# Kernel optimization log

Measured on AMD Instinct MI355X. Metric: run time of the kernel, lower is better.

## Reference

```python
import jax, jax.numpy as jnp
import numpy as np
import math

B, S, D = 4, 2048, 1024


def setup_inputs() -> dict:
    key = jax.random.key(0)
    k1, k2, k3 = jax.random.split(key, 3)
    X = jax.random.normal(k1, (B, S, D), dtype=jnp.float32)
    # causal mask, broadcast over batch (True = keep)
    mask = jnp.broadcast_to(jnp.tril(jnp.ones((S, S), dtype=bool)), (B, S, S))
    # torch nn.Linear weights: y = x @ W.T; init scale ~ 1/sqrt(D)
    WQK = jax.random.normal(k2, (D, D), dtype=jnp.float32) / math.sqrt(D)
    WOV = jax.random.normal(k3, (D, D), dtype=jnp.float32) / math.sqrt(D)
    return {"X": X, "mask": mask, "WQK": WQK, "WOV": WOV}


def reference(X, mask, WQK, WOV):
    d = X.shape[-1]
    Q = jnp.einsum('bsd,ed->bse', X, WQK)          # WQK(X) = X @ WQK.T
    Sc = jnp.einsum('bse,bte->bst', Q, X)          # shared-QK scores: Q @ X^T
    # NOTE: original multiplies by sqrt(d_model) (not divide) - faithful
    Sc = Sc * jnp.asarray(math.sqrt(d), Sc.dtype)
    Sc = jnp.where(mask, Sc, -jnp.inf)
    A = jax.nn.softmax(Sc, axis=-1)                # dropout p=0.0 -> identity
    V = jnp.einsum('bsd,ed->bse', X, WOV)          # WOV(X)
    Y = jnp.einsum('bst,bte->bse', A, V)
    return (X + Y, A)
```

## Files before the change

### kernel.cpp

```cpp
#include <hip/hip_runtime.h>
#include <hip/hip_fp16.h>
#include <math.h>

typedef _Float16 half_t;
typedef _Float16 h8_t __attribute__((ext_vector_type(8)));
typedef _Float16 h4_t __attribute__((ext_vector_type(4)));
typedef float f4_t __attribute__((ext_vector_type(4)));

#define MFMA16(a, b, c) __builtin_amdgcn_mfma_f32_16x16x32_f16(a, b, c, 0, 0, 0)

static constexpr int kB = 4;
static constexpr int kS = 2048;
static constexpr int kD = 1024;
static constexpr int BM = 128;
static constexpr int BN = 128;
static constexpr int BK = 32;
static constexpr int NT = 512;

__device__ __forceinline__ void gload16(const half_t* g, half_t* l) {
  __builtin_amdgcn_global_load_lds(
      (const __attribute__((address_space(1))) void*)g,
      (__attribute__((address_space(3))) void*)l, 16, 0, 0);
}

__device__ __forceinline__ void stage_tile(half_t* __restrict__ sm,
                                           const half_t* __restrict__ g, int ld) {
  const int t = threadIdx.x;
  const int r = t >> 2;
  const int c = ((t & 3) * 8) ^ ((((r >> 1) & 3)) << 3);
  gload16(&g[(size_t)r * ld + c], &sm[r * BK + (t & 3) * 8]);
}

template <bool SPLIT>
__device__ __forceinline__ void stage_all(half_t* buf, const half_t* Ahi,
                                          const half_t* Alo, int lda,
                                          const half_t* Bhi, const half_t* Blo,
                                          int ldb, size_t ko) {
  stage_tile(buf, Ahi + ko, lda);
  stage_tile(buf + BM * BK, Bhi + ko, ldb);
  if (SPLIT) {
    stage_tile(buf + 2 * BM * BK, Alo + ko, lda);
    stage_tile(buf + 3 * BM * BK, Blo + ko, ldb);
  }
}

template <bool SPLIT>
__device__ __forceinline__ void gemm_core(const half_t* __restrict__ Ahi,
                                          const half_t* __restrict__ Alo, int lda,
                                          const half_t* __restrict__ Bhi,
                                          const half_t* __restrict__ Blo, int ldb,
                                          int k_iters, half_t* sm, f4_t acc[4][2]) {
  constexpr int BUFSZ = (SPLIT ? 4 : 2) * BM * BK;
  const int lane = threadIdx.x & 63;
  const int wid = threadIdx.x >> 6;
  const int wm = (wid >> 2) * 64;
  const int wn = (wid & 3) * 32;
  const int fr = lane & 15;
  const int fk = (((lane >> 4) * 8) ^ (((lane >> 1) & 3) << 3));

  half_t* cur = sm;
  half_t* nxt = sm + BUFSZ;

  stage_all<SPLIT>(cur, Ahi, Alo, lda, Bhi, Blo, ldb, 0);
  asm volatile("s_waitcnt vmcnt(0)" ::: "memory");
  __builtin_amdgcn_s_barrier();

  for (int kk = 0; kk < k_iters; ++kk) {
    if (kk + 1 < k_iters)
      stage_all<SPLIT>(nxt, Ahi, Alo, lda, Bhi, Blo, ldb, (size_t)(kk + 1) * BK);
    const half_t* sAh = cur;
    const half_t* sBh = cur + BM * BK;
    const half_t* sAl = cur + 2 * BM * BK;
    const half_t* sBl = cur + 3 * BM * BK;
    h8_t a[4], b[2], al[4], bl[2];
#pragma unroll
    for (int i = 0; i < 4; ++i) {
      a[i] = *(const h8_t*)&sAh[(wm + i * 16 + fr) * BK + fk];
      if (SPLIT) al[i] = *(const h8_t*)&sAl[(wm + i * 16 + fr) * BK + fk];
    }
#pragma unroll
    for (int j = 0; j < 2; ++j) {
      b[j] = *(const h8_t*)&sBh[(wn + j * 16 + fr) * BK + fk];
      if (SPLIT) bl[j] = *(const h8_t*)&sBl[(wn + j * 16 + fr) * BK + fk];
    }
#pragma unroll
    for (int i = 0; i < 4; ++i)
#pragma unroll
      for (int j = 0; j < 2; ++j) {
        acc[i][j] = MFMA16(a[i], b[j], acc[i][j]);
        if (SPLIT) {
          acc[i][j] = MFMA16(a[i], bl[j], acc[i][j]);
          acc[i][j] = MFMA16(al[i], b[j], acc[i][j]);
        }
      }
    asm volatile("s_waitcnt vmcnt(0)" ::: "memory");
    __builtin_amdgcn_s_barrier();
    half_t* t = cur; cur = nxt; nxt = t;
  }
}

__global__ __launch_bounds__(NT) void gemm_q_kernel(
    const half_t* __restrict__ Xhi, const half_t* __restrict__ Xlo,
    const half_t* __restrict__ Whi, const half_t* __restrict__ Wlo,
    half_t* __restrict__ Qhi, half_t* __restrict__ Qlo) {
  __shared__ half_t sm[2 * 4 * BM * BK];
  const size_t arow = (size_t)blockIdx.y * BM;
  const size_t brow = (size_t)blockIdx.x * BN;
  f4_t acc[4][2] = {};
  gemm_core<true>(Xhi + arow * kD, Xlo + arow * kD, kD,
                  Whi + brow * kD, Wlo + brow * kD, kD, kD / BK, sm, acc);
  const int lane = threadIdx.x & 63;
  const int wid = threadIdx.x >> 6;
  const int wm = (wid >> 2) * 64, wn = (wid & 3) * 32;
  const int c16 = lane & 15, r4 = (lane >> 4) * 4;
#pragma unroll
  for (int i = 0; i < 4; ++i)
#pragma unroll
    for (int j = 0; j < 2; ++j)
#pragma unroll
      for (int r = 0; r < 4; ++r) {
        const size_t row = arow + wm + i * 16 + r4 + r;
        const size_t col = brow + wn + j * 16 + c16;
        const float q = acc[i][j][r];
        const half_t qh = (half_t)q;
        const half_t ql = (half_t)(q - (float)qh);
        const size_t idx = row * kD + col;
        Qhi[idx] = qh;
        Qlo[idx] = ql;
      }
}

__global__ __launch_bounds__(NT) void gemm_v_kernel(
    const half_t* __restrict__ Xhi, const half_t* __restrict__ Whi,
    half_t* __restrict__ Vt) {
  __shared__ half_t sm[2 * 2 * BM * BK];
  const size_t arow = (size_t)blockIdx.y * BM;
  const size_t brow = (size_t)blockIdx.x * BN;
  f4_t acc[4][2] = {};
  gemm_core<false>(Xhi + arow * kD, nullptr, kD, Whi + brow * kD, nullptr, kD,
                   kD / BK, sm, acc);
  const int lane = threadIdx.x & 63;
  const int wid = threadIdx.x >> 6;
  const int wm = (wid >> 2) * 64, wn = (wid & 3) * 32;
  const int c16 = lane & 15, r4 = (lane >> 4) * 4;
#pragma unroll
  for (int i = 0; i < 4; ++i)
#pragma unroll
    for (int j = 0; j < 2; ++j)
#pragma unroll
      for (int r = 0; r < 4; ++r) {
        const size_t row = arow + wm + i * 16 + r4 + r;
        const size_t col = brow + wn + j * 16 + c16;
        const size_t bi = row >> 11;
        const size_t s = row & 2047;
        Vt[bi * (size_t)kD * kS + col * kS + s] = (half_t)acc[i][j][r];
      }
}

__global__ __launch_bounds__(NT) void gemm_score_kernel(
    const half_t* __restrict__ Qhi, const half_t* __restrict__ Qlo,
    const half_t* __restrict__ Xhi, const half_t* __restrict__ Xlo,
    float* __restrict__ Sc) {
  const int tn = blockIdx.x, tm = blockIdx.y, bi = blockIdx.z;
  if (tn > tm) return;
  __shared__ half_t sm[2 * 4 * BM * BK];
  const size_t arow = (size_t)bi * kS + (size_t)tm * BM;
  const size_t brow = (size_t)bi * kS + (size_t)tn * BN;
  f4_t acc[4][2] = {};
  gemm_core<true>(Qhi + arow * kD, Qlo + arow * kD, kD,
                  Xhi + brow * kD, Xlo + brow * kD, kD, kD / BK, sm, acc);
  float* out = Sc + (size_t)bi * kS * kS;
  const int lane = threadIdx.x & 63;
  const int wid = threadIdx.x >> 6;
  const int wm = (wid >> 2) * 64, wn = (wid & 3) * 32;
  const int c16 = lane & 15, r4 = (lane >> 4) * 4;
#pragma unroll
  for (int i = 0; i < 4; ++i)
#pragma unroll
    for (int j = 0; j < 2; ++j)
#pragma unroll
      for (int r = 0; r < 4; ++r) {
        const int row = tm * BM + wm + i * 16 + r4 + r;
        const int col = tn * BN + wn + j * 16 + c16;
        out[(size_t)row * kS + col] = 32.0f * acc[i][j][r];
      }
}

__global__ __launch_bounds__(256) void softmax_kernel(float* __restrict__ A,
                                                      half_t* __restrict__ Ah) {
  const int rgl = blockIdx.x;
  const int s = rgl & 2047;
  float* row = A + (size_t)rgl * kS;
  half_t* hrow = Ah + (size_t)rgl * kS;
  const int tid = threadIdx.x;
  const int n = s + 1;
  float v[8];
  float mx = -INFINITY;
#pragma unroll
  for (int i = 0; i < 8; ++i) {
    const int t = tid + i * 256;
    v[i] = (t < n) ? row[t] : -INFINITY;
    mx = fmaxf(mx, v[i]);
  }
  for (int off = 32; off; off >>= 1) mx = fmaxf(mx, __shfl_xor(mx, off));
  __shared__ float red[8];
  const int lane = tid & 63, wid = tid >> 6;
  if (lane == 0) red[wid] = mx;
  __syncthreads();
  if (tid == 0) {
    float m = fmaxf(fmaxf(red[0], red[1]), fmaxf(red[2], red[3]));
    red[4] = m;
  }
  __syncthreads();
  mx = red[4];
  float sum = 0.0f;
#pragma unroll
  for (int i = 0; i < 8; ++i) {
    v[i] = (tid + i * 256 < n) ? __expf(v[i] - mx) : 0.0f;
    sum += v[i];
  }
  for (int off = 32; off; off >>= 1) sum += __shfl_xor(sum, off);
  __syncthreads();
  if (lane == 0) red[wid] = sum;
  __syncthreads();
  if (tid == 0) red[5] = 1.0f / (red[0] + red[1] + red[2] + red[3]);
  __syncthreads();
  const float inv = red[5];
#pragma unroll
  for (int i = 0; i < 8; ++i) {
    const int t = tid + i * 256;
    const float a = v[i] * inv;
    row[t] = a;
    hrow[t] = (half_t)a;
  }
}

__global__ __launch_bounds__(NT) void gemm_y_kernel(
    const half_t* __restrict__ Ah, const half_t* __restrict__ Vt,
    const float* __restrict__ X, float* __restrict__ Out) {
  __shared__ half_t sm[2 * 2 * BM * BK];
  const int tn = blockIdx.x, bi = blockIdx.z;
  const int tm = (kS / BM - 1) - blockIdx.y;
  const size_t abase = ((size_t)bi * kS + (size_t)tm * BM) * kS;
  const size_t bbase = ((size_t)bi * kD + (size_t)tn * BN) * kS;
  f4_t acc[4][2] = {};
  gemm_core<false>(Ah + abase, nullptr, kS, Vt + bbase, nullptr, kS,
                   (tm + 1) * BM / BK, sm, acc);
  const size_t obase = (size_t)bi * kS * kD;
  const int lane = threadIdx.x & 63;
  const int wid = threadIdx.x >> 6;
  const int wm = (wid >> 2) * 64, wn = (wid & 3) * 32;
  const int c16 = lane & 15, r4 = (lane >> 4) * 4;
#pragma unroll
  for (int i = 0; i < 4; ++i)
#pragma unroll
    for (int j = 0; j < 2; ++j)
#pragma unroll
      for (int r = 0; r < 4; ++r) {
        const size_t row = (size_t)tm * BM + wm + i * 16 + r4 + r;
        const size_t col = (size_t)tn * BN + wn + j * 16 + c16;
        const size_t idx = obase + row * kD + col;
        Out[idx] = X[idx] + acc[i][j][r];
      }
}

__global__ __launch_bounds__(256) void split_kernel(const float* __restrict__ x,
                                                    half_t* __restrict__ hi,
                                                    half_t* __restrict__ lo, int n4) {
  const int i = blockIdx.x * 256 + threadIdx.x;
  if (i >= n4) return;
  const float4 v = ((const float4*)x)[i];
  const float vv[4] = {v.x, v.y, v.z, v.w};
  h4_t h, l;
#pragma unroll
  for (int j = 0; j < 4; ++j) {
    const half_t hh = (half_t)vv[j];
    h[j] = hh;
    l[j] = (half_t)(vv[j] - (float)hh);
  }
  ((h4_t*)hi)[i] = h;
  ((h4_t*)lo)[i] = l;
}

__global__ __launch_bounds__(256) void cvt_kernel(const float* __restrict__ x,
                                                  half_t* __restrict__ hi, int n4) {
  const int i = blockIdx.x * 256 + threadIdx.x;
  if (i >= n4) return;
  const float4 v = ((const float4*)x)[i];
  h4_t h;
  h[0] = (half_t)v.x; h[1] = (half_t)v.y; h[2] = (half_t)v.z; h[3] = (half_t)v.w;
  ((h4_t*)hi)[i] = h;
}

extern "C" void kernel_launch(void* const* d_in, const int* in_sizes, int n_in,
                              void* d_out, int out_size, void* d_ws, size_t ws_size,
                              hipStream_t stream) {
  const float* X   = (const float*)d_in[0];
  const float* WQK = (const float*)d_in[2];
  const float* WOV = (const float*)d_in[3];

  constexpr size_t nX = (size_t)kB * kS * kD;
  constexpr size_t nW = (size_t)kD * kD;
  constexpr size_t nA = (size_t)kB * kS * kS;

  float* out0 = (float*)d_out;
  float* outA = out0 + nX;

  half_t* ws = (half_t*)d_ws;
  half_t* Xhi = ws; ws += nX;
  half_t* Xlo = ws; ws += nX;
  half_t* Qhi = ws; ws += nX;
  half_t* Qlo = ws; ws += nX;
  half_t* Whi = ws; ws += nW;
  half_t* Wlo = ws; ws += nW;
  half_t* WVh = ws; ws += nW;
  half_t* Vt  = ws; ws += nX;
  half_t* Ah  = ws; ws += nA;
  const size_t need_bytes = (size_t)((char*)ws - (char*)d_ws);
  if (ws_size < need_bytes) return;

  split_kernel<<<(int)(nX / 4 / 256), 256, 0, stream>>>(X, Xhi, Xlo, (int)(nX / 4));
  split_kernel<<<(int)(nW / 4 / 256), 256, 0, stream>>>(WQK, Whi, Wlo, (int)(nW / 4));
  cvt_kernel<<<(int)(nW / 4 / 256), 256, 0, stream>>>(WOV, WVh, (int)(nW / 4));

  gemm_q_kernel<<<dim3(kD / BN, kB * kS / BM), NT, 0, stream>>>(Xhi, Xlo, Whi, Wlo, Qhi, Qlo);
  gemm_v_kernel<<<dim3(kD / BN, kB * kS / BM), NT, 0, stream>>>(Xhi, WVh, Vt);
  gemm_score_kernel<<<dim3(kS / BN, kS / BM, kB), NT, 0, stream>>>(Qhi, Qlo, Xhi, Xlo, outA);
  softmax_kernel<<<kB * kS, 256, 0, stream>>>(outA, Ah);
  gemm_y_kernel<<<dim3(kD / BN, kS / BM, kB), NT, 0, stream>>>(Ah, Vt, X, out0);
}
```

Baseline: 380.0 us.

## Restructure GEMM mainloop with two-deep prefetch and register-prefetched A fragments

Rewrites the shared GEMM core so that two k-tiles are kept in flight. The next A fragments are loaded from LDS into registers while the current MFMAs run, and waits use partial vmcnt counts instead of draining all global loads each iteration. The main loop is unrolled by two with ping-pong register sets. Launch bounds now request 4 waves per SIMD, which may constrain register allocation and cause spills. The loop also assumes k_iters is even, and it adds a second barrier per step.

After: 382.3 us. No clear change (+0.6%).

```diff
diff --git a/kernel.cpp b/kernel.cpp
--- a/kernel.cpp
+++ b/kernel.cpp
@@ -45,11 +45,57 @@
 }
 
 template <bool SPLIT>
+__device__ __forceinline__ void kstep(int t, int k_iters, half_t* b0, half_t* b1,
+                                      const half_t* Ahi, const half_t* Alo, int lda,
+                                      const half_t* Bhi, const half_t* Blo, int ldb,
+                                      int wm, int wn, int fr, int fk,
+                                      h8_t (&a)[4], h8_t (&al)[4],
+                                      h8_t (&an)[4], h8_t (&aln)[4],
+                                      f4_t (&acc)[4][2]) {
+  half_t* bc = (t & 1) ? b1 : b0;
+  half_t* bn = (t & 1) ? b0 : b1;
+  h8_t b[2], bl[2];
+#pragma unroll
+  for (int j = 0; j < 2; ++j) {
+    b[j] = *(const h8_t*)&bc[BM * BK + (wn + j * 16 + fr) * BK + fk];
+    if (SPLIT) bl[j] = *(const h8_t*)&bc[3 * BM * BK + (wn + j * 16 + fr) * BK + fk];
+  }
+#pragma unroll
+  for (int i = 0; i < 4; ++i)
+#pragma unroll
+    for (int j = 0; j < 2; ++j) {
+      acc[i][j] = MFMA16(a[i], b[j], acc[i][j]);
+      if (SPLIT) {
+        acc[i][j] = MFMA16(a[i], bl[j], acc[i][j]);
+        acc[i][j] = MFMA16(al[i], b[j], acc[i][j]);
+      }
+    }
+  asm volatile("s_waitcnt lgkmcnt(0)" ::: "memory");
+  __builtin_amdgcn_s_barrier();
+  if (t + 2 < k_iters)
+    stage_all<SPLIT>(bc, Ahi, Alo, lda, Bhi, Blo, ldb, (size_t)(t + 2) * BK);
+  if (t + 1 < k_iters) {
+    if (t + 2 < k_iters) {
+      if (SPLIT) asm volatile("s_waitcnt vmcnt(4)" ::: "memory");
+      else       asm volatile("s_waitcnt vmcnt(2)" ::: "memory");
+    } else {
+      asm volatile("s_waitcnt vmcnt(0)" ::: "memory");
+    }
+    __builtin_amdgcn_s_barrier();
+#pragma unroll
+    for (int i = 0; i < 4; ++i) {
+      an[i] = *(const h8_t*)&bn[(wm + i * 16 + fr) * BK + fk];
+      if (SPLIT) aln[i] = *(const h8_t*)&bn[2 * BM * BK + (wm + i * 16 + fr) * BK + fk];
+    }
+  }
+}
+
+template <bool SPLIT>
 __device__ __forceinline__ void gemm_core(const half_t* __restrict__ Ahi,
                                           const half_t* __restrict__ Alo, int lda,
                                           const half_t* __restrict__ Bhi,
                                           const half_t* __restrict__ Blo, int ldb,
-                                          int k_iters, half_t* sm, f4_t acc[4][2]) {
+                                          int k_iters, half_t* sm, f4_t (&acc)[4][2]) {
   constexpr int BUFSZ = (SPLIT ? 4 : 2) * BM * BK;
   const int lane = threadIdx.x & 63;
   const int wid = threadIdx.x >> 6;
@@ -58,48 +104,31 @@
   const int fr = lane & 15;
   const int fk = (((lane >> 4) * 8) ^ (((lane >> 1) & 3) << 3));
 
-  half_t* cur = sm;
-  half_t* nxt = sm + BUFSZ;
-
-  stage_all<SPLIT>(cur, Ahi, Alo, lda, Bhi, Blo, ldb, 0);
-  asm volatile("s_waitcnt vmcnt(0)" ::: "memory");
+  half_t* b0 = sm;
+  half_t* b1 = sm + BUFSZ;
+
+  stage_all<SPLIT>(b0, Ahi, Alo, lda, Bhi, Blo, ldb, 0);
+  stage_all<SPLIT>(b1, Ahi, Alo, lda, Bhi, Blo, ldb, BK);
+  if (SPLIT) asm volatile("s_waitcnt vmcnt(4)" ::: "memory");
+  else       asm volatile("s_waitcnt vmcnt(2)" ::: "memory");
   __builtin_amdgcn_s_barrier();
 
-  for (int kk = 0; kk < k_iters; ++kk) {
-    if (kk + 1 < k_iters)
-      stage_all<SPLIT>(nxt, Ahi, Alo, lda, Bhi, Blo, ldb, (size_t)(kk + 1) * BK);
-    const half_t* sAh = cur;
-    const half_t* sBh = cur + BM * BK;
-    const half_t* sAl = cur + 2 * BM * BK;
-    const half_t* sBl = cur + 3 * BM * BK;
-    h8_t a[4], b[2], al[4], bl[2];
-#pragma unroll
-    for (int i = 0; i < 4; ++i) {
-      a[i] = *(const h8_t*)&sAh[(wm + i * 16 + fr) * BK + fk];
-      if (SPLIT) al[i] = *(const h8_t*)&sAl[(wm + i * 16 + fr) * BK + fk];
-    }
-#pragma unroll
-    for (int j = 0; j < 2; ++j) {
-      b[j] = *(const h8_t*)&sBh[(wn + j * 16 + fr) * BK + fk];
-      if (SPLIT) bl[j] = *(const h8_t*)&sBl[(wn + j * 16 + fr) * BK + fk];
-    }
-#pragma unroll
-    for (int i = 0; i < 4; ++i)
-#pragma unroll
-      for (int j = 0; j < 2; ++j) {
-        acc[i][j] = MFMA16(a[i], b[j], acc[i][j]);
-        if (SPLIT) {
-          acc[i][j] = MFMA16(a[i], bl[j], acc[i][j]);
-          acc[i][j] = MFMA16(al[i], b[j], acc[i][j]);
-        }
-      }
-    asm volatile("s_waitcnt vmcnt(0)" ::: "memory");
-    __builtin_amdgcn_s_barrier();
-    half_t* t = cur; cur = nxt; nxt = t;
-  }
-}
-
-__global__ __launch_bounds__(NT) void gemm_q_kernel(
+  h8_t a[4], al[4], an[4], aln[4];
+#pragma unroll
+  for (int i = 0; i < 4; ++i) {
+    a[i] = *(const h8_t*)&b0[(wm + i * 16 + fr) * BK + fk];
+    if (SPLIT) al[i] = *(const h8_t*)&b0[2 * BM * BK + (wm + i * 16 + fr) * BK + fk];
+  }
+
+  for (int t = 0; t < k_iters; t += 2) {
+    kstep<SPLIT>(t,     k_iters, b0, b1, Ahi, Alo, lda, Bhi, Blo, ldb,
+                 wm, wn, fr, fk, a, al, an, aln, acc);
+    kstep<SPLIT>(t + 1, k_iters, b0, b1, Ahi, Alo, lda, Bhi, Blo, ldb,
+                 wm, wn, fr, fk, an, aln, a, al, acc);
+  }
+}
+
+__global__ __launch_bounds__(NT, 4) void gemm_q_kernel(
     const half_t* __restrict__ Xhi, const half_t* __restrict__ Xlo,
     const half_t* __restrict__ Whi, const half_t* __restrict__ Wlo,
     half_t* __restrict__ Qhi, half_t* __restrict__ Qlo) {
@@ -130,7 +159,7 @@
       }
 }
 
-__global__ __launch_bounds__(NT) void gemm_v_kernel(
+__global__ __launch_bounds__(NT, 4) void gemm_v_kernel(
     const half_t* __restrict__ Xhi, const half_t* __restrict__ Whi,
     half_t* __restrict__ Vt) {
   __shared__ half_t sm[2 * 2 * BM * BK];
@@ -157,7 +186,7 @@
       }
 }
 
-__global__ __launch_bounds__(NT) void gemm_score_kernel(
+__global__ __launch_bounds__(NT, 4) void gemm_score_kernel(
     const half_t* __restrict__ Qhi, const half_t* __restrict__ Qlo,
     const half_t* __restrict__ Xhi, const half_t* __restrict__ Xlo,
     float* __restrict__ Sc) {
@@ -235,7 +264,7 @@
   }
 }
 
-__global__ __launch_bounds__(NT) void gemm_y_kernel(
+__global__ __launch_bounds__(NT, 4) void gemm_y_kernel(
     const half_t* __restrict__ Ah, const half_t* __restrict__ Vt,
     const float* __restrict__ X, float* __restrict__ Out) {
   __shared__ half_t sm[2 * 2 * BM * BK];
```
